# Optimization experiments

Hardware: AMD Instinct MI355X
Metric: run time of the kernel (lower is better)

The kernel has to match this reference:

```python
import jax, jax.numpy as jnp
import numpy as np

B, I, C, U, S = 256, 128, 1024, 32, 16  # batch, in_units, in_channels, num_units, unit_size
NUM_ITERS = 3

def setup_inputs() -> dict:
    key = jax.random.key(0)
    k1, k2 = jax.random.split(key)
    x = jax.random.normal(k1, (B, I, C), dtype=jnp.float32)
    W = jax.random.normal(k2, (1, C, U, S, I), dtype=jnp.float32)
    return {"x": x, "W": W}

def _squash(s):
    # s: (b, u, s); original squashes over dim=2 of (b,1,U,S,1), i.e. the num_units axis
    mag_sq = jnp.sum(s * s, axis=1, keepdims=True)
    mag = jnp.sqrt(mag_sq)
    return mag_sq / (1.0 + mag_sq) * (s / mag)

def reference(x, W):
    # x: (b, in_units, in_channels) -> (b, c, i)
    xT = jnp.swapaxes(x, 1, 2)
    # u_hat[b,c,u,s] = sum_i W[0,c,u,s,i] * xT[b,c,i]  (replaces torch.cat broadcast + matmul)
    u_hat = jnp.einsum('cusi,bci->bcus', W[0], xT)
    b_ij = jnp.zeros((1, C, U, 1), dtype=x.dtype)
    v_j = None
    for _ in range(NUM_ITERS):
        # softmax over axis 0 of size 1 -> all ones (faithful to original quirk)
        c_ij = jax.nn.softmax(b_ij, axis=0)
        s_j = jnp.einsum('cu,bcus->bus', c_ij[0, :, :, 0], u_hat)
        v_j = _squash(s_j)
        # agreement: mean over batch of <u_hat, v_j> along unit_size
        u_vj = jnp.einsum('bcus,bus->cu', u_hat, v_j) / B
        b_ij = b_ij + u_vj[None, :, :, None]
    return v_j[..., None]  # (b, num_units, unit_size, 1) == v_j.squeeze(1)
```

## Files before the change

### kernel.cpp

```cpp
#include <hip/hip_runtime.h>
#include <hip/hip_bf16.h>
#include <stdint.h>

#define B_DIM 256
#define I_DIM 128
#define C_DIM 1024
#define N_DIM 512
#define KC    (C_DIM * I_DIM)
#define WC    (N_DIM * I_DIM)
#define BI    (B_DIM * I_DIM)

typedef __bf16 bf16;
typedef __attribute__((ext_vector_type(8))) __bf16 bf16x8;
typedef __attribute__((ext_vector_type(4))) float f32x4;

__device__ __forceinline__ void async_copy16(const void* g, void* l) {
  __builtin_amdgcn_global_load_lds(
      (const __attribute__((address_space(1))) uint32_t*)g,
      (__attribute__((address_space(3))) uint32_t*)l, 16, 0, 0);
}

__global__ void __launch_bounds__(256)
transpose_cast(const float* __restrict__ x, bf16* __restrict__ xc) {
  __shared__ float tile[64][65];
  const int c0 = blockIdx.x * 64;
  const int i0 = blockIdx.y * 64;
  const int b  = blockIdx.z;
  const int t  = threadIdx.x;
  const int sub = t >> 4;
  const int cg  = t & 15;
  const float* xb = x + (size_t)b * (I_DIM * C_DIM);
#pragma unroll
  for (int r = 0; r < 4; ++r) {
    const int i = r * 16 + sub;
    const float4 v = *(const float4*)&xb[(size_t)(i0 + i) * C_DIM + c0 + cg * 4];
    tile[i][cg * 4 + 0] = v.x; tile[i][cg * 4 + 1] = v.y;
    tile[i][cg * 4 + 2] = v.z; tile[i][cg * 4 + 3] = v.w;
  }
  __syncthreads();
#pragma unroll
  for (int r = 0; r < 2; ++r) {
    const int c  = r * 32 + (t >> 3);
    const int ic = (t & 7) * 8;
    bf16x8 o;
#pragma unroll
    for (int k = 0; k < 8; ++k) o[k] = (bf16)tile[ic + k][c];
    *(bf16x8*)&xc[(size_t)(c0 + c) * BI + (size_t)b * I_DIM + i0 + ic] = o;
  }
}

__device__ __forceinline__ void stage_step(
    const bf16* __restrict__ xc, const float* __restrict__ W,
    short* Asl, float* Wsl, int tid, int c, int h, int n0) {
  const size_t abase = (size_t)c * BI + h * 64;
#pragma unroll
  for (int p = 0; p < 4; ++p) {
    const int g  = p * 512 + tid;
    const int b  = g >> 3;
    const int cs = (g & 7) ^ (b & 7);
    async_copy16(xc + abase + (size_t)b * I_DIM + cs * 8, Asl + (size_t)g * 8);
  }
  const size_t wbase = (size_t)c * WC + (size_t)n0 * I_DIM + h * 64;
#pragma unroll
  for (int p = 0; p < 4; ++p) {
    const int g  = p * 512 + tid;
    const int n  = g >> 4;
    const int qs = (g & 15) ^ (n & 15);
    async_copy16(W + wbase + (size_t)n * I_DIM + qs * 4, Wsl + (size_t)g * 4);
  }
}

__device__ __forceinline__ void compute_step(
    const short* As, const float* Wl,
    int wm, int wn2, int l15, int lq, f32x4 (&acc)[8][2]) {
  const int m7 = l15 & 7;
#pragma unroll
  for (int ksl = 0; ksl < 2; ++ksl) {
    bf16x8 a[8];
#pragma unroll
    for (int mt = 0; mt < 8; ++mt) {
      const int m  = wm * 128 + mt * 16 + l15;
      const int st = (ksl * 4 + lq) ^ m7;
      a[mt] = *(const bf16x8*)&As[m * 64 + st * 8];
    }
    bf16x8 b[2];
#pragma unroll
    for (int nt = 0; nt < 2; ++nt) {
      const int n  = wn2 * 32 + nt * 16 + l15;
      const int q0 = ksl * 8 + lq * 2;
      const f32x4 lo = *(const f32x4*)&Wl[n * 64 + ((q0 ^ l15) * 4)];
      const f32x4 hi = *(const f32x4*)&Wl[n * 64 + (((q0 + 1) ^ l15) * 4)];
      bf16x8 bb;
      bb[0] = (bf16)lo[0]; bb[1] = (bf16)lo[1];
      bb[2] = (bf16)lo[2]; bb[3] = (bf16)lo[3];
      bb[4] = (bf16)hi[0]; bb[5] = (bf16)hi[1];
      bb[6] = (bf16)hi[2]; bb[7] = (bf16)hi[3];
      b[nt] = bb;
    }
#pragma unroll
    for (int mt = 0; mt < 8; ++mt)
#pragma unroll
      for (int nt = 0; nt < 2; ++nt)
        acc[mt][nt] = __builtin_amdgcn_mfma_f32_16x16x32_bf16(
            a[mt], b[nt], acc[mt][nt], 0, 0, 0);
  }
}

__global__ void __launch_bounds__(512, 2)
gemm_kernel(const bf16* __restrict__ xc, const float* __restrict__ W,
            float* __restrict__ sj) {
  __shared__ short As[2][B_DIM * 64];
  __shared__ float Wl[2][128 * 64];
  const int tid  = threadIdx.x;
  const int lane = tid & 63;
  const int wv   = tid >> 6;
  const int wm   = wv >> 2;
  const int wn2  = wv & 3;
  const int l15  = lane & 15;
  const int lq   = lane >> 4;

  const int g     = blockIdx.x;
  const int chunk = (g & 7) * 8 + ((g >> 3) & 7);
  const int nb    = g >> 6;
  const int n0    = nb * 128;
  const int c0    = chunk * 16;

  f32x4 acc[8][2] = {};

  stage_step(xc, W, As[0], Wl[0], tid, c0, 0, n0);

#pragma unroll 1
  for (int t = 0; t < 31; ++t) {
    const int tn = t + 1;
    stage_step(xc, W, As[tn & 1], Wl[tn & 1], tid, c0 + (tn >> 1), tn & 1, n0);
    asm volatile("s_waitcnt vmcnt(8)" ::: "memory");
    __builtin_amdgcn_sched_barrier(0);
    __builtin_amdgcn_s_barrier();
    compute_step(As[t & 1], Wl[t & 1], wm, wn2, l15, lq, acc);
    __builtin_amdgcn_s_barrier();
  }
  asm volatile("s_waitcnt vmcnt(0)" ::: "memory");
  __builtin_amdgcn_sched_barrier(0);
  __builtin_amdgcn_s_barrier();
  compute_step(As[1], Wl[1], wm, wn2, l15, lq, acc);

#pragma unroll
  for (int mt = 0; mt < 8; ++mt) {
#pragma unroll
    for (int nt = 0; nt < 2; ++nt) {
      const int n = n0 + wn2 * 32 + nt * 16 + l15;
#pragma unroll
      for (int r = 0; r < 4; ++r) {
        const int brow = wm * 128 + mt * 16 + lq * 4 + r;
        atomicAdd(&sj[(size_t)brow * N_DIM + n], acc[mt][nt][r]);
      }
    }
  }
}

__global__ void __launch_bounds__(512)
squash_kernel(const float* __restrict__ sj, float* __restrict__ out) {
  __shared__ float sm[512];
  const int b = blockIdx.x;
  const int t = threadIdx.x;
  const float v = sj[(size_t)b * N_DIM + t];
  sm[t] = v * v;
  __syncthreads();
#pragma unroll
  for (int off = 256; off >= 16; off >>= 1) {
    if (t < off) sm[t] += sm[t + off];
    __syncthreads();
  }
  const float msq   = sm[t & 15];
  const float scale = sqrtf(msq) / (1.0f + msq);
  out[(size_t)b * N_DIM + t] = v * scale;
}

extern "C" void kernel_launch(void* const* d_in, const int* in_sizes, int n_in,
                              void* d_out, int out_size, void* d_ws, size_t ws_size,
                              hipStream_t stream) {
  const float* x = (const float*)d_in[0];
  const float* W = (const float*)d_in[1];
  float* out = (float*)d_out;

  bf16*  xc = (bf16*)d_ws;
  float* sj = (float*)((char*)d_ws + (size_t)KC * B_DIM * sizeof(bf16));

  hipMemsetAsync(sj, 0, (size_t)B_DIM * N_DIM * sizeof(float), stream);
  transpose_cast<<<dim3(C_DIM / 64, I_DIM / 64, B_DIM), 256, 0, stream>>>(x, xc);
  gemm_kernel<<<dim3(256), 512, 0, stream>>>(xc, W, sj);
  squash_kernel<<<B_DIM, 512, 0, stream>>>(sj, out);
}
```

Baseline: 477.9 us.

## Retile GEMM to 128x64 output blocks over 64-channel chunks with full-K steps

Each GEMM block now computes a 128-row by 64-column output tile over 64 input channels, instead of 256x128 over 16 channels. Each pipeline step stages the full 128-wide i dimension for one channel, so the loop runs 64 steps instead of 32, and the LDS swizzles are redone for the new row widths. Each wave now holds a 2x2 set of MFMA accumulators instead of 8x2, which lowers register pressure and spreads the reduction over more channels per block. The cost is that each W element is now fetched by two batch blocks and each x element by eight column blocks, roughly doubling global or L2 traffic. Each MFMA also gets less operand reuse from LDS.

```diff
diff --git a/kernel.cpp b/kernel.cpp
--- a/kernel.cpp
+++ b/kernel.cpp
@@ -51,45 +51,45 @@
 
 __device__ __forceinline__ void stage_step(
     const bf16* __restrict__ xc, const float* __restrict__ W,
-    short* Asl, float* Wsl, int tid, int c, int h, int n0) {
-  const size_t abase = (size_t)c * BI + h * 64;
+    short* Asl, float* Wsl, int tid, int c, int mb, int n0) {
+  const size_t abase = (size_t)c * BI + (size_t)(mb * 128) * I_DIM;
 #pragma unroll
   for (int p = 0; p < 4; ++p) {
     const int g  = p * 512 + tid;
-    const int b  = g >> 3;
-    const int cs = (g & 7) ^ (b & 7);
-    async_copy16(xc + abase + (size_t)b * I_DIM + cs * 8, Asl + (size_t)g * 8);
+    const int b  = g >> 4;
+    const int ch = (g & 15) ^ (b & 7);
+    async_copy16(xc + abase + (size_t)b * I_DIM + ch * 8, Asl + (size_t)g * 8);
   }
-  const size_t wbase = (size_t)c * WC + (size_t)n0 * I_DIM + h * 64;
+  const size_t wbase = (size_t)c * WC + (size_t)n0 * I_DIM;
 #pragma unroll
   for (int p = 0; p < 4; ++p) {
-    const int g  = p * 512 + tid;
-    const int n  = g >> 4;
-    const int qs = (g & 15) ^ (n & 15);
-    async_copy16(W + wbase + (size_t)n * I_DIM + qs * 4, Wsl + (size_t)g * 4);
+    const int g = p * 512 + tid;
+    const int n = g >> 5;
+    const int q = (g & 31) ^ (n & 7);
+    async_copy16(W + wbase + (size_t)n * I_DIM + q * 4, Wsl + (size_t)g * 4);
   }
 }
 
 __device__ __forceinline__ void compute_step(
     const short* As, const float* Wl,
-    int wm, int wn2, int l15, int lq, f32x4 (&acc)[8][2]) {
-  const int m7 = l15 & 7;
+    int wm, int wn, int l15, int lq, f32x4 (&acc)[2][2]) {
 #pragma unroll
-  for (int ksl = 0; ksl < 2; ++ksl) {
-    bf16x8 a[8];
+  for (int ksl = 0; ksl < 4; ++ksl) {
+    bf16x8 a[2];
 #pragma unroll
-    for (int mt = 0; mt < 8; ++mt) {
-      const int m  = wm * 128 + mt * 16 + l15;
-      const int st = (ksl * 4 + lq) ^ m7;
-      a[mt] = *(const bf16x8*)&As[m * 64 + st * 8];
+    for (int mt = 0; mt < 2; ++mt) {
+      const int m  = wm * 32 + mt * 16 + l15;
+      const int ch = (ksl * 4 + lq) ^ (m & 7);
+      a[mt] = *(const bf16x8*)&As[m * 128 + ch * 8];
     }
     bf16x8 b[2];
 #pragma unroll
     for (int nt = 0; nt < 2; ++nt) {
-      const int n  = wn2 * 32 + nt * 16 + l15;
-      const int q0 = ksl * 8 + lq * 2;
-      const f32x4 lo = *(const f32x4*)&Wl[n * 64 + ((q0 ^ l15) * 4)];
-      const f32x4 hi = *(const f32x4*)&Wl[n * 64 + (((q0 + 1) ^ l15) * 4)];
+      const int n  = wn * 32 + nt * 16 + l15;
+      const int q0 = (ksl * 8 + lq * 2)     ^ (n & 7);
+      const int q1 = (ksl * 8 + lq * 2 + 1) ^ (n & 7);
+      const f32x4 lo = *(const f32x4*)&Wl[n * 128 + q0 * 4];
+      const f32x4 hi = *(const f32x4*)&Wl[n * 128 + q1 * 4];
       bf16x8 bb;
       bb[0] = (bf16)lo[0]; bb[1] = (bf16)lo[1];
       bb[2] = (bf16)lo[2]; bb[3] = (bf16)lo[3];
@@ -98,7 +98,7 @@
       b[nt] = bb;
     }
 #pragma unroll
-    for (int mt = 0; mt < 8; ++mt)
+    for (int mt = 0; mt < 2; ++mt)
 #pragma unroll
       for (int nt = 0; nt < 2; ++nt)
         acc[mt][nt] = __builtin_amdgcn_mfma_f32_16x16x32_bf16(
@@ -109,49 +109,51 @@
 __global__ void __launch_bounds__(512, 2)
 gemm_kernel(const bf16* __restrict__ xc, const float* __restrict__ W,
             float* __restrict__ sj) {
-  __shared__ short As[2][B_DIM * 64];
-  __shared__ float Wl[2][128 * 64];
+  __shared__ short As[2][128 * I_DIM];
+  __shared__ float Wl[2][64 * I_DIM];
   const int tid  = threadIdx.x;
   const int lane = tid & 63;
   const int wv   = tid >> 6;
-  const int wm   = wv >> 2;
-  const int wn2  = wv & 3;
+  const int wm   = wv & 3;
+  const int wn   = wv >> 2;
   const int l15  = lane & 15;
   const int lq   = lane >> 4;
 
   const int g     = blockIdx.x;
-  const int chunk = (g & 7) * 8 + ((g >> 3) & 7);
-  const int nb    = g >> 6;
-  const int n0    = nb * 128;
-  const int c0    = chunk * 16;
+  const int s     = g >> 3;
+  const int chunk = (g & 7) + 8 * (s >> 4);
+  const int mb    = (s >> 3) & 1;
+  const int nb    = s & 7;
+  const int n0    = nb * 64;
+  const int c0    = chunk * 64;
 
-  f32x4 acc[8][2] = {};
+  f32x4 acc[2][2] = {};
 
-  stage_step(xc, W, As[0], Wl[0], tid, c0, 0, n0);
+  stage_step(xc, W, As[0], Wl[0], tid, c0, mb, n0);
 
 #pragma unroll 1
-  for (int t = 0; t < 31; ++t) {
+  for (int t = 0; t < 63; ++t) {
     const int tn = t + 1;
-    stage_step(xc, W, As[tn & 1], Wl[tn & 1], tid, c0 + (tn >> 1), tn & 1, n0);
+    stage_step(xc, W, As[tn & 1], Wl[tn & 1], tid, c0 + tn, mb, n0);
     asm volatile("s_waitcnt vmcnt(8)" ::: "memory");
     __builtin_amdgcn_sched_barrier(0);
     __builtin_amdgcn_s_barrier();
-    compute_step(As[t & 1], Wl[t & 1], wm, wn2, l15, lq, acc);
+    compute_step(As[t & 1], Wl[t & 1], wm, wn, l15, lq, acc);
     __builtin_amdgcn_s_barrier();
   }
   asm volatile("s_waitcnt vmcnt(0)" ::: "memory");
   __builtin_amdgcn_sched_barrier(0);
   __builtin_amdgcn_s_barrier();
-  compute_step(As[1], Wl[1], wm, wn2, l15, lq, acc);
+  compute_step(As[1], Wl[1], wm, wn, l15, lq, acc);
 
 #pragma unroll
-  for (int mt = 0; mt < 8; ++mt) {
+  for (int mt = 0; mt < 2; ++mt) {
 #pragma unroll
     for (int nt = 0; nt < 2; ++nt) {
-      const int n = n0 + wn2 * 32 + nt * 16 + l15;
+      const int n = n0 + wn * 32 + nt * 16 + l15;
 #pragma unroll
       for (int r = 0; r < 4; ++r) {
-        const int brow = wm * 128 + mt * 16 + lq * 4 + r;
+        const int brow = mb * 128 + wm * 32 + mt * 16 + lq * 4 + r;
         atomicAdd(&sj[(size_t)brow * N_DIM + n], acc[mt][nt][r]);
       }
     }
```

Result: slower. 501.0 us (+4.8%).

## Load A fragments directly into registers and stage full-K W tiles in LDS

Applied to the files above, without the earlier changes.

The GEMM no longer stages the x operand through LDS. Each wave now loads its own 32 batch rows straight from global memory into registers, double-buffered across channels. W is staged for the full 128-wide K per channel, and the loop steps one channel at a time instead of half-channels, which halves the number of barriers. Each wave now computes a 32x128 tile instead of 128x32, so each W fragment converted from LDS is reused by only 2 MFMAs. This adds more LDS reads and fp32-to-bf16 conversions per MFMA, raises register pressure, and exposes the direct global loads' latency.

```diff
diff --git a/kernel.cpp b/kernel.cpp
--- a/kernel.cpp
+++ b/kernel.cpp
@@ -49,73 +49,62 @@
   }
 }
 
-__device__ __forceinline__ void stage_step(
-    const bf16* __restrict__ xc, const float* __restrict__ W,
-    short* Asl, float* Wsl, int tid, int c, int h, int n0) {
-  const size_t abase = (size_t)c * BI + h * 64;
+__device__ __forceinline__ void stage_W(const float* __restrict__ W,
+                                        float* Wsl, int tid, int c, int n0) {
+  const float* base = W + (size_t)c * WC + (size_t)n0 * I_DIM;
 #pragma unroll
-  for (int p = 0; p < 4; ++p) {
-    const int g  = p * 512 + tid;
-    const int b  = g >> 3;
-    const int cs = (g & 7) ^ (b & 7);
-    async_copy16(xc + abase + (size_t)b * I_DIM + cs * 8, Asl + (size_t)g * 8);
-  }
-  const size_t wbase = (size_t)c * WC + (size_t)n0 * I_DIM + h * 64;
-#pragma unroll
-  for (int p = 0; p < 4; ++p) {
-    const int g  = p * 512 + tid;
-    const int n  = g >> 4;
-    const int qs = (g & 15) ^ (n & 15);
-    async_copy16(W + wbase + (size_t)n * I_DIM + qs * 4, Wsl + (size_t)g * 4);
+  for (int p = 0; p < 8; ++p) {
+    const int G = p * 512 + tid;
+    const int n = G >> 5;
+    const int s = G & 31;
+    const int q = s ^ (n & 15);
+    async_copy16(base + (size_t)n * I_DIM + q * 4, Wsl + (size_t)G * 4);
   }
 }
 
-__device__ __forceinline__ void compute_step(
-    const short* As, const float* Wl,
-    int wm, int wn2, int l15, int lq, f32x4 (&acc)[8][2]) {
-  const int m7 = l15 & 7;
+__device__ __forceinline__ void load_A(const bf16* __restrict__ xc, int c,
+                                       int wb, int l15, int lq,
+                                       bf16x8 (&a)[2][4]) {
+  const bf16* Ab = xc + (size_t)c * BI + (size_t)wb * I_DIM;
 #pragma unroll
-  for (int ksl = 0; ksl < 2; ++ksl) {
-    bf16x8 a[8];
+  for (int mt = 0; mt < 2; ++mt)
 #pragma unroll
-    for (int mt = 0; mt < 8; ++mt) {
-      const int m  = wm * 128 + mt * 16 + l15;
-      const int st = (ksl * 4 + lq) ^ m7;
-      a[mt] = *(const bf16x8*)&As[m * 64 + st * 8];
-    }
-    bf16x8 b[2];
+    for (int ks = 0; ks < 4; ++ks)
+      a[mt][ks] = *(const bf16x8*)&Ab[(mt * 16 + l15) * I_DIM + ks * 32 + lq * 8];
+}
+
+__device__ __forceinline__ void compute_step(const bf16x8 (&a)[2][4],
+    const float* Wsl, int l15, int lq, f32x4 (&acc)[2][8]) {
 #pragma unroll
-    for (int nt = 0; nt < 2; ++nt) {
-      const int n  = wn2 * 32 + nt * 16 + l15;
-      const int q0 = ksl * 8 + lq * 2;
-      const f32x4 lo = *(const f32x4*)&Wl[n * 64 + ((q0 ^ l15) * 4)];
-      const f32x4 hi = *(const f32x4*)&Wl[n * 64 + (((q0 + 1) ^ l15) * 4)];
+  for (int ks = 0; ks < 4; ++ks) {
+#pragma unroll
+    for (int nt = 0; nt < 8; ++nt) {
+      const int n  = nt * 16 + l15;
+      const int f  = l15;
+      const int qd = ks * 8 + lq * 2;
+      const f32x4 lo = *(const f32x4*)&Wsl[n * I_DIM + ((qd)     ^ f) * 4];
+      const f32x4 hi = *(const f32x4*)&Wsl[n * I_DIM + ((qd + 1) ^ f) * 4];
       bf16x8 bb;
       bb[0] = (bf16)lo[0]; bb[1] = (bf16)lo[1];
       bb[2] = (bf16)lo[2]; bb[3] = (bf16)lo[3];
       bb[4] = (bf16)hi[0]; bb[5] = (bf16)hi[1];
       bb[6] = (bf16)hi[2]; bb[7] = (bf16)hi[3];
-      b[nt] = bb;
+#pragma unroll
+      for (int mt = 0; mt < 2; ++mt)
+        acc[mt][nt] = __builtin_amdgcn_mfma_f32_16x16x32_bf16(
+            a[mt][ks], bb, acc[mt][nt], 0, 0, 0);
     }
-#pragma unroll
-    for (int mt = 0; mt < 8; ++mt)
-#pragma unroll
-      for (int nt = 0; nt < 2; ++nt)
-        acc[mt][nt] = __builtin_amdgcn_mfma_f32_16x16x32_bf16(
-            a[mt], b[nt], acc[mt][nt], 0, 0, 0);
   }
 }
 
 __global__ void __launch_bounds__(512, 2)
 gemm_kernel(const bf16* __restrict__ xc, const float* __restrict__ W,
             float* __restrict__ sj) {
-  __shared__ short As[2][B_DIM * 64];
-  __shared__ float Wl[2][128 * 64];
+  __shared__ float Wl[2][128 * I_DIM];
   const int tid  = threadIdx.x;
   const int lane = tid & 63;
-  const int wv   = tid >> 6;
-  const int wm   = wv >> 2;
-  const int wn2  = wv & 3;
+  const int wave = tid >> 6;
+  const int wb   = wave * 32;
   const int l15  = lane & 15;
   const int lq   = lane >> 4;
 
@@ -125,33 +114,49 @@
   const int n0    = nb * 128;
   const int c0    = chunk * 16;
 
-  f32x4 acc[8][2] = {};
+  f32x4  acc[2][8] = {};
+  bf16x8 aA[2][4], aB[2][4];
 
-  stage_step(xc, W, As[0], Wl[0], tid, c0, 0, n0);
+  load_A(xc, c0, wb, l15, lq, aA);
+  stage_W(W, Wl[0], tid, c0, n0);
 
 #pragma unroll 1
-  for (int t = 0; t < 31; ++t) {
-    const int tn = t + 1;
-    stage_step(xc, W, As[tn & 1], Wl[tn & 1], tid, c0 + (tn >> 1), tn & 1, n0);
-    asm volatile("s_waitcnt vmcnt(8)" ::: "memory");
+  for (int j = 0; j < 7; ++j) {
+    const int t0 = 2 * j;
+    load_A(xc, c0 + t0 + 1, wb, l15, lq, aB);
+    stage_W(W, Wl[1], tid, c0 + t0 + 1, n0);
+    asm volatile("s_waitcnt vmcnt(16)" ::: "memory");
     __builtin_amdgcn_sched_barrier(0);
     __builtin_amdgcn_s_barrier();
-    compute_step(As[t & 1], Wl[t & 1], wm, wn2, l15, lq, acc);
+    compute_step(aA, Wl[0], l15, lq, acc);
+    __builtin_amdgcn_s_barrier();
+    load_A(xc, c0 + t0 + 2, wb, l15, lq, aA);
+    stage_W(W, Wl[0], tid, c0 + t0 + 2, n0);
+    asm volatile("s_waitcnt vmcnt(16)" ::: "memory");
+    __builtin_amdgcn_sched_barrier(0);
+    __builtin_amdgcn_s_barrier();
+    compute_step(aB, Wl[1], l15, lq, acc);
     __builtin_amdgcn_s_barrier();
   }
+  load_A(xc, c0 + 15, wb, l15, lq, aB);
+  stage_W(W, Wl[1], tid, c0 + 15, n0);
+  asm volatile("s_waitcnt vmcnt(16)" ::: "memory");
+  __builtin_amdgcn_sched_barrier(0);
+  __builtin_amdgcn_s_barrier();
+  compute_step(aA, Wl[0], l15, lq, acc);
   asm volatile("s_waitcnt vmcnt(0)" ::: "memory");
   __builtin_amdgcn_sched_barrier(0);
   __builtin_amdgcn_s_barrier();
-  compute_step(As[1], Wl[1], wm, wn2, l15, lq, acc);
+  compute_step(aB, Wl[1], l15, lq, acc);
 
 #pragma unroll
-  for (int mt = 0; mt < 8; ++mt) {
+  for (int mt = 0; mt < 2; ++mt) {
 #pragma unroll
-    for (int nt = 0; nt < 2; ++nt) {
-      const int n = n0 + wn2 * 32 + nt * 16 + l15;
+    for (int nt = 0; nt < 8; ++nt) {
+      const int n = n0 + nt * 16 + l15;
 #pragma unroll
       for (int r = 0; r < 4; ++r) {
-        const int brow = wm * 128 + mt * 16 + lq * 4 + r;
+        const int brow = wb + mt * 16 + lq * 4 + r;
         atomicAdd(&sj[(size_t)brow * N_DIM + n], acc[mt][nt][r]);
       }
     }
```

Result: slower. 526.3 us (+10.1%).
